# Optimization experiments

Measured on AMD Instinct MI355X. Metric: run time of the kernel, lower is better.

## Reference

```python
import jax, jax.numpy as jnp
import numpy as np

B, N, C, H = 8, 1024, 1024, 16
D = C // H
SCALE = D ** -0.5


def setup_inputs() -> dict:
    key = jax.random.key(0)
    ks = jax.random.split(key, 5)
    s = 0.02  # keep pre-softmax logits in a sane range
    return {
        "x": jax.random.normal(ks[0], (B, N, C), dtype=jnp.float32),
        "Wq": jax.random.normal(ks[1], (C, C), dtype=jnp.float32) * s,
        "bq": jax.random.normal(ks[2], (C,), dtype=jnp.float32) * s,
        "Wkv": jax.random.normal(ks[3], (C, 2 * C), dtype=jnp.float32) * s,
        "bkv": jax.random.normal(ks[4], (2 * C,), dtype=jnp.float32) * s,
    }


def reference(x, Wq, bq, Wkv, bkv):
    b, n, c = x.shape
    h, d = H, c // H
    q = (x @ Wq + bq).reshape(b, n, h, d)                 # [b,n,h,d]
    kv = x @ Wkv + bkv                                     # [b,n,2c]
    k, v = jnp.split(kv, 2, axis=-1)                       # each [b,n,c]
    k = k.reshape(b, n, h, d)
    v = v.reshape(b, n, h, d)
    att = jnp.einsum("bnhd,bmhd->bnmh", q, k) * SCALE      # [b,n,m,h]
    att = jax.nn.softmax(att, axis=2)                      # softmax over keys (m)
    out = jnp.einsum("bnmh,bmhd->bnhd", att, v).reshape(b, n, c)
    return out
```

## Files before the change

### kernel.cpp

```cpp
#include <hip/hip_runtime.h>
#include <stdint.h>

using u16 = unsigned short;
using u32 = unsigned int;
using bf16x8 = __attribute__((ext_vector_type(8))) __bf16;
using f32x4  = __attribute__((ext_vector_type(4))) float;

#define NB 8
#define NN 1024
#define NC 1024
#define NH 16
#define ND 64
#define QSCALE 0.18033688011112042f

__device__ __forceinline__ u16 f2bf(float f) {
  u32 u = __float_as_uint(f);
  return (u16)((u + 0x7fffu + ((u >> 16) & 1u)) >> 16);
}
__device__ __forceinline__ u16 bfc(float f) {
  __bf16 b = (__bf16)f;
  return __builtin_bit_cast(u16, b);
}
__device__ __forceinline__ u32 pack2(u16 a, u16 b) { return (u32)a | ((u32)b << 16); }

__device__ __forceinline__ void gload16(const void* g, void* l) {
  __builtin_amdgcn_global_load_lds((__attribute__((address_space(1))) const u32*)g,
                                   (__attribute__((address_space(3))) u32*)l, 16, 0, 0);
}

__global__ void k_prep(const float* __restrict__ x, const float* __restrict__ Wq,
                       const float* __restrict__ bq, const float* __restrict__ Wkv,
                       const float* __restrict__ bkv,
                       u16* __restrict__ xb, u16* __restrict__ Wt, float* __restrict__ bias) {
  __shared__ u16 tile[64][72];
  int bid = blockIdx.x;
  int t = threadIdx.x;
  if (bid < 8192) {
    int i = bid * 256 + t;
    float4 v = ((const float4*)x)[i];
    ((uint2*)xb)[i] = make_uint2(pack2(f2bf(v.x), f2bf(v.y)), pack2(f2bf(v.z), f2bf(v.w)));
    return;
  }
  if (bid < 8960) {
    int pb = bid - 8192;
    int k0 = (pb & 15) << 6;
    int c0 = (pb >> 4) << 6;
    bool isQ = (c0 < 1024);
    const float* src = isQ ? Wq : Wkv;
    int ldw  = isQ ? 1024 : 2048;
    int csrc = isQ ? c0 : (c0 - 1024);
    float sc = isQ ? QSCALE : 1.0f;

    int r  = t >> 2;
    int cq = (t & 3) << 4;
    const float* p = src + (size_t)(k0 + r) * ldw + csrc + cq;
#pragma unroll
    for (int j = 0; j < 16; j += 4) {
      float4 v = *(const float4*)(p + j);
      tile[r][cq + j + 0] = f2bf(v.x * sc);
      tile[r][cq + j + 1] = f2bf(v.y * sc);
      tile[r][cq + j + 2] = f2bf(v.z * sc);
      tile[r][cq + j + 3] = f2bf(v.w * sc);
    }
    __syncthreads();
    int co = t >> 2;
    int kq = (t & 3) << 4;
    u16 v0[16];
#pragma unroll
    for (int j = 0; j < 16; ++j) v0[j] = tile[kq + j][co];
    uint4 o0, o1;
    o0.x = pack2(v0[0], v0[1]);  o0.y = pack2(v0[2], v0[3]);
    o0.z = pack2(v0[4], v0[5]);  o0.w = pack2(v0[6], v0[7]);
    o1.x = pack2(v0[8], v0[9]);  o1.y = pack2(v0[10], v0[11]);
    o1.z = pack2(v0[12], v0[13]); o1.w = pack2(v0[14], v0[15]);
    u16* dst = Wt + (size_t)(c0 + co) * 1024 + k0 + kq;
    *(uint4*)dst = o0;
    *(uint4*)(dst + 8) = o1;
    return;
  }
  {
    int i = (bid - 8960) * 256 + t;
    if (i < 1024) bias[i] = bq[i] * QSCALE;
    else if (i < 3072) bias[i] = bkv[i - 1024];
  }
}

__launch_bounds__(512, 4)
__global__ void k_gemm(const u16* __restrict__ A, const u16* __restrict__ Bw,
                       const float* __restrict__ bias,
                       u16* __restrict__ qws, u16* __restrict__ kws, u16* __restrict__ vtw) {
  __shared__ __align__(16) u16 Ab[2][4096];
  __shared__ __align__(16) u16 Bb[2][8192];
  int flat = blockIdx.x;
  int swz = (flat & 7) * 96 + (flat >> 3);
  int m0 = (swz & 63) * 128;
  int n0 = (swz >> 6) * 256;
  int tid = threadIdx.x;
  int w = tid >> 6, lane = tid & 63;
  int lo = lane & 15, hi = lane >> 4;
  int wm = w >> 2, wn = w & 3;

  f32x4 acc[4][4] = {};

  int srow = tid >> 2;
  int schunk = (tid & 3) ^ ((tid >> 3) & 3);
  const u16* Ag  = A  + (size_t)(m0 + srow) * 1024 + schunk * 8;
  const u16* Bg0 = Bw + (size_t)(n0 + srow) * 1024 + schunk * 8;
  const u16* Bg1 = Bw + (size_t)(n0 + 128 + srow) * 1024 + schunk * 8;

  int ck = ((hi ^ ((lo >> 1) & 3)) << 3);

#define STAGE(BUF, KO)                                  \
  gload16(Ag  + (KO), &Ab[BUF][tid * 8]);               \
  gload16(Bg0 + (KO), &Bb[BUF][tid * 8]);               \
  gload16(Bg1 + (KO), &Bb[BUF][4096 + tid * 8]);

  STAGE(0, 0);
  __syncthreads();

  for (int t = 0; t < 32; ++t) {
    int cb = t & 1;
    if (t < 31) { STAGE(cb ^ 1, (t + 1) * 32); }
    bf16x8 af[4], bfr[4];
#pragma unroll
    for (int mi = 0; mi < 4; ++mi)
      af[mi] = *(const bf16x8*)&Ab[cb][(wm * 64 + mi * 16 + lo) * 32 + ck];
#pragma unroll
    for (int ni = 0; ni < 4; ++ni)
      bfr[ni] = *(const bf16x8*)&Bb[cb][(wn * 64 + ni * 16 + lo) * 32 + ck];
#pragma unroll
    for (int mi = 0; mi < 4; ++mi)
#pragma unroll
      for (int ni = 0; ni < 4; ++ni)
        acc[mi][ni] = __builtin_amdgcn_mfma_f32_16x16x32_bf16(af[mi], bfr[ni], acc[mi][ni], 0, 0, 0);
    __syncthreads();
  }
#undef STAGE

#pragma unroll
  for (int ni = 0; ni < 4; ++ni) {
    int c = n0 + wn * 64 + ni * 16 + lo;
    float bvl = bias[c];
    if (c < 2048) {
#pragma unroll
      for (int mi = 0; mi < 4; ++mi) {
#pragma unroll
        for (int r = 0; r < 4; ++r) {
          int m = m0 + wm * 64 + mi * 16 + hi * 4 + r;
          int b = m >> 10, tok = m & 1023;
          u16 o = f2bf(acc[mi][ni][r] + bvl);
          if (c < 1024) {
            int h = c >> 6, d = c & 63;
            qws[((size_t)(b * 16 + h) * 1024 + tok) * 64 + d] = o;
          } else {
            int c2 = c - 1024; int h = c2 >> 6, d = c2 & 63;
            kws[((size_t)(b * 16 + h) * 1024 + tok) * 64 + d] = o;
          }
        }
      }
    } else {
      int c2 = c - 2048; int h = c2 >> 6, d = c2 & 63;
#pragma unroll
      for (int mi = 0; mi < 4; ++mi) {
        int m = m0 + wm * 64 + mi * 16 + hi * 4;
        int b = m >> 10, tok = m & 1023;
        ushort4 pk;
        pk.x = bfc(acc[mi][ni][0] + bvl);
        pk.y = bfc(acc[mi][ni][1] + bvl);
        pk.z = bfc(acc[mi][ni][2] + bvl);
        pk.w = bfc(acc[mi][ni][3] + bvl);
        *(ushort4*)&vtw[((size_t)(b * 16 + h) * 64 + d) * 1024 + tok] = pk;
      }
    }
  }
}

__launch_bounds__(512)
__global__ void k_attn(const u16* __restrict__ q, const u16* __restrict__ k,
                       const u16* __restrict__ vt, float* __restrict__ out) {
  __shared__ __align__(16) u16 Ks[2][4096];
  __shared__ __align__(16) u16 Vs[2][4096];
  __shared__ __align__(16) u16 P[8][16][72];
  int bh = blockIdx.x;
  int q0 = blockIdx.y * 128;
  int tid = threadIdx.x;
  int w = tid >> 6, lane = tid & 63;
  int lo = lane & 15, hi = lane >> 4;
  int b = bh >> 4, h = bh & 15;

  const u16* kbase = k  + (size_t)bh * 65536;
  const u16* vbase = vt + (size_t)bh * 65536;

  int srow = w * 8 + (lane >> 3);
  int cg   = (lane & 7) ^ ((lane >> 3) & 7);
  const u16* gK = kbase + (size_t)srow * 64   + cg * 8;
  const u16* gV = vbase + (size_t)srow * 1024 + cg * 8;
  u16* lK0 = &Ks[0][w * 512];
  u16* lK1 = &Ks[1][w * 512];
  u16* lV0 = &Vs[0][w * 512];
  u16* lV1 = &Vs[1][w * 512];

  const u16* qp = q + ((size_t)bh * 1024 + q0 + w * 16 + lo) * 64 + hi * 8;
  bf16x8 qf0 = *(const bf16x8*)(qp);
  bf16x8 qf1 = *(const bf16x8*)(qp + 32);

  f32x4 acc_o[4] = {};
  float m_s = -1e30f;
  float l_s = 0.f;

  int sw = lo & 7;

  gload16(gK, lK0);
  gload16(gV, lV0);
  __syncthreads();

  for (int t = 0; t < 16; ++t) {
    int cur = t & 1;
    if (t < 15) {
      gload16(gK + (t + 1) * 4096, cur ? lK0 : lK1);
      gload16(gV + (t + 1) * 64,   cur ? lV0 : lV1);
    }
    f32x4 s[4] = {};
    const u16* kb = Ks[cur];
#pragma unroll
    for (int ni = 0; ni < 4; ++ni) {
      const u16* kp = kb + (ni * 16 + lo) * 64;
      bf16x8 kf0 = *(const bf16x8*)(kp + ((hi ^ sw) * 8));
      bf16x8 kf1 = *(const bf16x8*)(kp + (((4 + hi) ^ sw) * 8));
      s[ni] = __builtin_amdgcn_mfma_f32_16x16x32_bf16(kf0, qf0, s[ni], 0, 0, 0);
      s[ni] = __builtin_amdgcn_mfma_f32_16x16x32_bf16(kf1, qf1, s[ni], 0, 0, 0);
    }
    float pm;
    {
      float a0 = fmaxf(fmaxf(s[0][0], s[0][1]), fmaxf(s[0][2], s[0][3]));
      float a1 = fmaxf(fmaxf(s[1][0], s[1][1]), fmaxf(s[1][2], s[1][3]));
      float a2 = fmaxf(fmaxf(s[2][0], s[2][1]), fmaxf(s[2][2], s[2][3]));
      float a3 = fmaxf(fmaxf(s[3][0], s[3][1]), fmaxf(s[3][2], s[3][3]));
      pm = fmaxf(fmaxf(a0, a1), fmaxf(a2, a3));
      pm = fmaxf(pm, __shfl_xor(pm, 16));
      pm = fmaxf(pm, __shfl_xor(pm, 32));
    }
    if (!__all(pm <= m_s + 8.0f)) {
      float mn = fmaxf(m_s, pm);
      float corr = __builtin_amdgcn_exp2f(m_s - mn);
      m_s = mn;
      l_s *= corr;
      float cr[4];
#pragma unroll
      for (int r = 0; r < 4; ++r) cr[r] = __shfl(corr, hi * 4 + r);
#pragma unroll
      for (int ci = 0; ci < 4; ++ci)
#pragma unroll
        for (int r = 0; r < 4; ++r) acc_o[ci][r] *= cr[r];
    }
    float rs = 0.f;
#pragma unroll
    for (int ni = 0; ni < 4; ++ni) {
      float p0 = __builtin_amdgcn_exp2f(s[ni][0] - m_s);
      float p1 = __builtin_amdgcn_exp2f(s[ni][1] - m_s);
      float p2 = __builtin_amdgcn_exp2f(s[ni][2] - m_s);
      float p3 = __builtin_amdgcn_exp2f(s[ni][3] - m_s);
      rs += (p0 + p1) + (p2 + p3);
      ushort4 pk;
      pk.x = bfc(p0); pk.y = bfc(p1); pk.z = bfc(p2); pk.w = bfc(p3);
      *(ushort4*)&P[w][lo][ni * 16 + hi * 4] = pk;
    }
    rs += __shfl_xor(rs, 16);
    rs += __shfl_xor(rs, 32);
    l_s += rs;
    bf16x8 pf0 = *(const bf16x8*)(&P[w][lo][hi * 8]);
    bf16x8 pf1 = *(const bf16x8*)(&P[w][lo][32 + hi * 8]);
    const u16* vb = Vs[cur];
#pragma unroll
    for (int ci = 0; ci < 4; ++ci) {
      const u16* vp = vb + (ci * 16 + lo) * 64;
      bf16x8 vf0 = *(const bf16x8*)(vp + ((hi ^ sw) * 8));
      bf16x8 vf1 = *(const bf16x8*)(vp + (((4 + hi) ^ sw) * 8));
      acc_o[ci] = __builtin_amdgcn_mfma_f32_16x16x32_bf16(pf0, vf0, acc_o[ci], 0, 0, 0);
      acc_o[ci] = __builtin_amdgcn_mfma_f32_16x16x32_bf16(pf1, vf1, acc_o[ci], 0, 0, 0);
    }
    __syncthreads();
  }
  float inv = 1.0f / l_s;
  float ivr[4];
#pragma unroll
  for (int r = 0; r < 4; ++r) ivr[r] = __shfl(inv, hi * 4 + r);
#pragma unroll
  for (int r = 0; r < 4; ++r) {
    int n = q0 + w * 16 + hi * 4 + r;
    float* dst = out + ((size_t)(b * 1024 + n)) * 1024 + h * 64;
#pragma unroll
    for (int ci = 0; ci < 4; ++ci) dst[ci * 16 + lo] = acc_o[ci][r] * ivr[r];
  }
}

extern "C" void kernel_launch(void* const* d_in, const int* in_sizes, int n_in,
                              void* d_out, int out_size, void* d_ws, size_t ws_size,
                              hipStream_t stream) {
  const float* x   = (const float*)d_in[0];
  const float* Wq  = (const float*)d_in[1];
  const float* bq  = (const float*)d_in[2];
  const float* Wkv = (const float*)d_in[3];
  const float* bkv = (const float*)d_in[4];
  float* out = (float*)d_out;

  char* ws = (char*)d_ws;
  u16*   xb   = (u16*)(ws);
  u16*   Wt   = (u16*)(ws + 16777216);
  float* bias = (float*)(ws + 23068672);
  u16*   qws  = (u16*)(ws + 23080960);
  u16*   kws  = (u16*)(ws + 39858176);
  u16*   vtw  = (u16*)(ws + 73412608);

  k_prep<<<8972, 256, 0, stream>>>(x, Wq, bq, Wkv, bkv, xb, Wt, bias);
  k_gemm<<<768, 512, 0, stream>>>(xb, Wt, bias, qws, kws, vtw);
  {
    dim3 g(128, 8);
    k_attn<<<g, 512, 0, stream>>>(qws, kws, vtw, out);
  }
}
```

Measured before the change: 139.4 us.

## Triple-buffer projection GEMM with split-phase loads, barriers and MFMA priority

Replaces the double-buffered K-loop of the QKV projection GEMM with a three-stage LDS ring. Each K-tile is split into two MFMA halves, with the A and B global loads for a later tile issued between them. Explicit vmcnt waits, s_barrier plus sched_barrier, and s_setprio around MFMA bursts aim to overlap global-to-LDS traffic with matrix math and let waves interleave better. The cost is 50% more LDS per block, which may reduce resident blocks per CU, plus more barriers per tile.

```diff
diff --git a/kernel.cpp b/kernel.cpp
--- a/kernel.cpp
+++ b/kernel.cpp
@@ -89,8 +89,8 @@
 __global__ void k_gemm(const u16* __restrict__ A, const u16* __restrict__ Bw,
                        const float* __restrict__ bias,
                        u16* __restrict__ qws, u16* __restrict__ kws, u16* __restrict__ vtw) {
-  __shared__ __align__(16) u16 Ab[2][4096];
-  __shared__ __align__(16) u16 Bb[2][8192];
+  __shared__ __align__(16) u16 RA[3][4096];
+  __shared__ __align__(16) u16 RB[3][8192];
   int flat = blockIdx.x;
   int swz = (flat & 7) * 96 + (flat >> 3);
   int m0 = (swz & 63) * 128;
@@ -110,32 +110,68 @@
 
   int ck = ((hi ^ ((lo >> 1) & 3)) << 3);
 
-#define STAGE(BUF, KO)                                  \
-  gload16(Ag  + (KO), &Ab[BUF][tid * 8]);               \
-  gload16(Bg0 + (KO), &Bb[BUF][tid * 8]);               \
-  gload16(Bg1 + (KO), &Bb[BUF][4096 + tid * 8]);
-
-  STAGE(0, 0);
-  __syncthreads();
-
-  for (int t = 0; t < 32; ++t) {
-    int cb = t & 1;
-    if (t < 31) { STAGE(cb ^ 1, (t + 1) * 32); }
-    bf16x8 af[4], bfr[4];
-#pragma unroll
-    for (int mi = 0; mi < 4; ++mi)
-      af[mi] = *(const bf16x8*)&Ab[cb][(wm * 64 + mi * 16 + lo) * 32 + ck];
-#pragma unroll
-    for (int ni = 0; ni < 4; ++ni)
-      bfr[ni] = *(const bf16x8*)&Bb[cb][(wn * 64 + ni * 16 + lo) * 32 + ck];
-#pragma unroll
-    for (int mi = 0; mi < 4; ++mi)
-#pragma unroll
-      for (int ni = 0; ni < 4; ++ni)
-        acc[mi][ni] = __builtin_amdgcn_mfma_f32_16x16x32_bf16(af[mi], bfr[ni], acc[mi][ni], 0, 0, 0);
-    __syncthreads();
-  }
-#undef STAGE
+#define MFMA_(a, b, c) __builtin_amdgcn_mfma_f32_16x16x32_bf16(a, b, c, 0, 0, 0)
+#define SBAR() __builtin_amdgcn_s_barrier(); __builtin_amdgcn_sched_barrier(0)
+
+#define TILE(S, SN, DOST, KT, VM0)                                            \
+  {                                                                           \
+    bf16x8 af[4], bfr[4];                                                     \
+    if (DOST) gload16(Ag + (size_t)(KT) * 32, &RA[SN][tid * 8]);              \
+    _Pragma("unroll")                                                         \
+    for (int mi = 0; mi < 4; ++mi)                                            \
+      af[mi] = *(const bf16x8*)&RA[S][(wm * 64 + mi * 16 + lo) * 32 + ck];    \
+    _Pragma("unroll")                                                         \
+    for (int ni = 0; ni < 2; ++ni)                                            \
+      bfr[ni] = *(const bf16x8*)&RB[S][(wn * 64 + ni * 16 + lo) * 32 + ck];   \
+    SBAR();                                                                   \
+    __builtin_amdgcn_s_setprio(1);                                            \
+    _Pragma("unroll")                                                         \
+    for (int mi = 0; mi < 4; ++mi)                                            \
+      _Pragma("unroll")                                                       \
+      for (int ni = 0; ni < 2; ++ni)                                          \
+        acc[mi][ni] = MFMA_(af[mi], bfr[ni], acc[mi][ni]);                    \
+    __builtin_amdgcn_s_setprio(0);                                            \
+    SBAR();                                                                   \
+    if (DOST) {                                                               \
+      gload16(Bg0 + (size_t)(KT) * 32, &RB[SN][tid * 8]);                     \
+      gload16(Bg1 + (size_t)(KT) * 32, &RB[SN][4096 + tid * 8]);              \
+    }                                                                         \
+    _Pragma("unroll")                                                         \
+    for (int ni = 2; ni < 4; ++ni)                                            \
+      bfr[ni] = *(const bf16x8*)&RB[S][(wn * 64 + ni * 16 + lo) * 32 + ck];   \
+    if (VM0) { asm volatile("s_waitcnt vmcnt(0)" ::: "memory"); }             \
+    else     { asm volatile("s_waitcnt vmcnt(3)" ::: "memory"); }             \
+    SBAR();                                                                   \
+    __builtin_amdgcn_s_setprio(1);                                            \
+    _Pragma("unroll")                                                         \
+    for (int mi = 0; mi < 4; ++mi)                                            \
+      _Pragma("unroll")                                                       \
+      for (int ni = 2; ni < 4; ++ni)                                          \
+        acc[mi][ni] = MFMA_(af[mi], bfr[ni], acc[mi][ni]);                    \
+    __builtin_amdgcn_s_setprio(0);                                            \
+    SBAR();                                                                   \
+  }
+
+  gload16(Ag,       &RA[0][tid * 8]);
+  gload16(Bg0,      &RB[0][tid * 8]);
+  gload16(Bg1,      &RB[0][4096 + tid * 8]);
+  gload16(Ag + 32,  &RA[1][tid * 8]);
+  gload16(Bg0 + 32, &RB[1][tid * 8]);
+  gload16(Bg1 + 32, &RB[1][4096 + tid * 8]);
+  asm volatile("s_waitcnt vmcnt(3)" ::: "memory");
+  SBAR();
+
+#pragma unroll 1
+  for (int u = 0; u < 30; u += 3) {
+    TILE(0, 2, true, u + 2, false);
+    TILE(1, 0, true, u + 3, false);
+    TILE(2, 1, true, u + 4, false);
+  }
+  TILE(0, 2, false, 0, true);
+  TILE(1, 0, false, 0, false);
+#undef TILE
+#undef SBAR
+#undef MFMA_
 
 #pragma unroll
   for (int ni = 0; ni < 4; ++ni) {
```

Result: no change. 139.1 us (-0.2%).

## Enlarge QKV GEMM tile to 256x256 with K=64 staging and interleaved MFMA schedule

Applied to the files above, without the earlier changes.

The projection GEMM moves from 128x256 tiles with K=32 steps to 256x256 tiles with K=64 steps, halving the grid to 384 blocks and doubling each wave's accumulator footprint. Global-to-LDS loads for the next tiles are interleaved between four MFMA quadrants, with explicit barriers, lgkm/vmcnt waits and s_setprio to overlap memory with compute. The aim is more reuse per loaded byte and fewer loop iterations and barriers. The cost is heavier register and LDS pressure (occupancy hint drops to 2) and only 384 blocks to spread across the CUs.

```diff
diff --git a/kernel.cpp b/kernel.cpp
--- a/kernel.cpp
+++ b/kernel.cpp
@@ -85,57 +85,136 @@
   }
 }
 
-__launch_bounds__(512, 4)
+__launch_bounds__(512, 2)
 __global__ void k_gemm(const u16* __restrict__ A, const u16* __restrict__ Bw,
                        const float* __restrict__ bias,
                        u16* __restrict__ qws, u16* __restrict__ kws, u16* __restrict__ vtw) {
-  __shared__ __align__(16) u16 Ab[2][4096];
-  __shared__ __align__(16) u16 Bb[2][8192];
+  __shared__ __align__(16) u16 LA[2][16384];
+  __shared__ __align__(16) u16 LB[2][16384];
   int flat = blockIdx.x;
-  int swz = (flat & 7) * 96 + (flat >> 3);
-  int m0 = (swz & 63) * 128;
-  int n0 = (swz >> 6) * 256;
+  int swz = (flat & 7) * 48 + (flat >> 3);
+  int m0 = (swz & 31) * 256;
+  int n0 = (swz >> 5) * 256;
   int tid = threadIdx.x;
   int w = tid >> 6, lane = tid & 63;
   int lo = lane & 15, hi = lane >> 4;
   int wm = w >> 2, wn = w & 3;
 
-  f32x4 acc[4][4] = {};
-
-  int srow = tid >> 2;
-  int schunk = (tid & 3) ^ ((tid >> 3) & 3);
-  const u16* Ag  = A  + (size_t)(m0 + srow) * 1024 + schunk * 8;
-  const u16* Bg0 = Bw + (size_t)(n0 + srow) * 1024 + schunk * 8;
-  const u16* Bg1 = Bw + (size_t)(n0 + 128 + srow) * 1024 + schunk * 8;
-
-  int ck = ((hi ^ ((lo >> 1) & 3)) << 3);
-
-#define STAGE(BUF, KO)                                  \
-  gload16(Ag  + (KO), &Ab[BUF][tid * 8]);               \
-  gload16(Bg0 + (KO), &Bb[BUF][tid * 8]);               \
-  gload16(Bg1 + (KO), &Bb[BUF][4096 + tid * 8]);
-
-  STAGE(0, 0);
-  __syncthreads();
-
-  for (int t = 0; t < 32; ++t) {
-    int cb = t & 1;
-    if (t < 31) { STAGE(cb ^ 1, (t + 1) * 32); }
-    bf16x8 af[4], bfr[4];
-#pragma unroll
-    for (int mi = 0; mi < 4; ++mi)
-      af[mi] = *(const bf16x8*)&Ab[cb][(wm * 64 + mi * 16 + lo) * 32 + ck];
-#pragma unroll
-    for (int ni = 0; ni < 4; ++ni)
-      bfr[ni] = *(const bf16x8*)&Bb[cb][(wn * 64 + ni * 16 + lo) * 32 + ck];
-#pragma unroll
-    for (int mi = 0; mi < 4; ++mi)
-#pragma unroll
-      for (int ni = 0; ni < 4; ++ni)
-        acc[mi][ni] = __builtin_amdgcn_mfma_f32_16x16x32_bf16(af[mi], bfr[ni], acc[mi][ni], 0, 0, 0);
-    __syncthreads();
-  }
-#undef STAGE
+  f32x4 acc[8][4] = {};
+
+  int cs = ((tid & 7) ^ ((tid >> 3) & 7)) * 8;
+  const u16* Ag = A  + (size_t)(m0 + (tid >> 3)) * 1024 + cs;
+  const u16* Bg = Bw + (size_t)(n0 + (tid >> 3)) * 1024 + cs;
+
+  int ck0 = ((hi ^ (lo & 7)) << 3);
+  int ck1 = (((4 + hi) ^ (lo & 7)) << 3);
+  const u16* laR = &LA[0][wm * 8192 + lo * 64];
+  const u16* lbR = &LB[0][(wn >> 1) * 8192 + ((wn & 1) * 64 + lo) * 64];
+
+#define MFMA_(a, b, c) __builtin_amdgcn_mfma_f32_16x16x32_bf16(a, b, c, 0, 0, 0)
+#define SBAR() __builtin_amdgcn_sched_barrier(0); __builtin_amdgcn_s_barrier(); __builtin_amdgcn_sched_barrier(0)
+#define LGKM0() asm volatile("s_waitcnt lgkmcnt(0)" ::: "memory"); __builtin_amdgcn_sched_barrier(0)
+
+#define ST_A(BUF, MH, KT)                                                                   \
+  gload16(Ag + (size_t)((MH) * 128) * 1024 + (KT) * 64,      &LA[BUF][(MH) * 8192 + tid * 8]); \
+  gload16(Ag + (size_t)((MH) * 128 + 64) * 1024 + (KT) * 64, &LA[BUF][(MH) * 8192 + 4096 + tid * 8]);
+#define ST_B(BUF, NH, KT)                                                                   \
+  gload16(Bg + (size_t)((NH) * 128) * 1024 + (KT) * 64,      &LB[BUF][(NH) * 8192 + tid * 8]); \
+  gload16(Bg + (size_t)((NH) * 128 + 64) * 1024 + (KT) * 64, &LB[BUF][(NH) * 8192 + 4096 + tid * 8]);
+
+  ST_A(0, 0, 0); ST_A(0, 1, 0); ST_B(0, 0, 0); ST_B(0, 1, 0);
+  ST_A(1, 0, 1); ST_A(1, 1, 1); ST_B(1, 0, 1);
+  asm volatile("s_waitcnt vmcnt(6)" ::: "memory");
+  __builtin_amdgcn_s_barrier();
+
+#pragma unroll 1
+  for (int t = 0; t < 16; ++t) {
+    int b = t & 1;
+    const u16* la = laR + b * 16384;
+    const u16* lb = lbR + b * 16384;
+    bf16x8 af[4][2], bf0[2][2], bf1[2][2];
+
+#pragma unroll
+    for (int mi = 0; mi < 4; ++mi) {
+      af[mi][0] = *(const bf16x8*)(la + mi * 1024 + ck0);
+      af[mi][1] = *(const bf16x8*)(la + mi * 1024 + ck1);
+    }
+#pragma unroll
+    for (int ni = 0; ni < 2; ++ni) {
+      bf0[ni][0] = *(const bf16x8*)(lb + ni * 1024 + ck0);
+      bf0[ni][1] = *(const bf16x8*)(lb + ni * 1024 + ck1);
+    }
+    if (t < 15) { ST_B(b ^ 1, 1, t + 1); }
+    SBAR();
+    LGKM0();
+    __builtin_amdgcn_s_setprio(1);
+#pragma unroll
+    for (int ks = 0; ks < 2; ++ks)
+#pragma unroll
+      for (int mi = 0; mi < 4; ++mi)
+#pragma unroll
+        for (int ni = 0; ni < 2; ++ni)
+          acc[mi][ni] = MFMA_(af[mi][ks], bf0[ni][ks], acc[mi][ni]);
+    __builtin_amdgcn_s_setprio(0);
+    SBAR();
+
+#pragma unroll
+    for (int ni = 0; ni < 2; ++ni) {
+      bf1[ni][0] = *(const bf16x8*)(lb + (2 + ni) * 1024 + ck0);
+      bf1[ni][1] = *(const bf16x8*)(lb + (2 + ni) * 1024 + ck1);
+    }
+    SBAR();
+    LGKM0();
+    __builtin_amdgcn_s_setprio(1);
+#pragma unroll
+    for (int ks = 0; ks < 2; ++ks)
+#pragma unroll
+      for (int mi = 0; mi < 4; ++mi)
+#pragma unroll
+        for (int ni = 0; ni < 2; ++ni)
+          acc[mi][2 + ni] = MFMA_(af[mi][ks], bf1[ni][ks], acc[mi][2 + ni]);
+    __builtin_amdgcn_s_setprio(0);
+    SBAR();
+
+#pragma unroll
+    for (int mi = 0; mi < 4; ++mi) {
+      af[mi][0] = *(const bf16x8*)(la + (4 + mi) * 1024 + ck0);
+      af[mi][1] = *(const bf16x8*)(la + (4 + mi) * 1024 + ck1);
+    }
+    if (t < 14) { ST_B(b, 0, t + 2); }
+    SBAR();
+    LGKM0();
+    __builtin_amdgcn_s_setprio(1);
+#pragma unroll
+    for (int ks = 0; ks < 2; ++ks)
+#pragma unroll
+      for (int mi = 0; mi < 4; ++mi)
+#pragma unroll
+        for (int ni = 0; ni < 2; ++ni)
+          acc[4 + mi][ni] = MFMA_(af[mi][ks], bf0[ni][ks], acc[4 + mi][ni]);
+    __builtin_amdgcn_s_setprio(0);
+    SBAR();
+
+    if (t < 14) { ST_A(b, 0, t + 2); ST_A(b, 1, t + 2); }
+    SBAR();
+    __builtin_amdgcn_s_setprio(1);
+#pragma unroll
+    for (int ks = 0; ks < 2; ++ks)
+#pragma unroll
+      for (int mi = 0; mi < 4; ++mi)
+#pragma unroll
+        for (int ni = 0; ni < 2; ++ni)
+          acc[4 + mi][2 + ni] = MFMA_(af[mi][ks], bf1[ni][ks], acc[4 + mi][2 + ni]);
+    __builtin_amdgcn_s_setprio(0);
+    if (t < 14)       { asm volatile("s_waitcnt vmcnt(6)" ::: "memory"); }
+    else if (t == 14) { asm volatile("s_waitcnt vmcnt(0)" ::: "memory"); }
+    SBAR();
+  }
+#undef ST_A
+#undef ST_B
+#undef SBAR
+#undef LGKM0
+#undef MFMA_
 
 #pragma unroll
   for (int ni = 0; ni < 4; ++ni) {
@@ -143,10 +222,10 @@
     float bvl = bias[c];
     if (c < 2048) {
 #pragma unroll
-      for (int mi = 0; mi < 4; ++mi) {
+      for (int mi = 0; mi < 8; ++mi) {
 #pragma unroll
         for (int r = 0; r < 4; ++r) {
-          int m = m0 + wm * 64 + mi * 16 + hi * 4 + r;
+          int m = m0 + wm * 128 + mi * 16 + hi * 4 + r;
           int b = m >> 10, tok = m & 1023;
           u16 o = f2bf(acc[mi][ni][r] + bvl);
           if (c < 1024) {
@@ -161,8 +240,8 @@
     } else {
       int c2 = c - 2048; int h = c2 >> 6, d = c2 & 63;
 #pragma unroll
-      for (int mi = 0; mi < 4; ++mi) {
-        int m = m0 + wm * 64 + mi * 16 + hi * 4;
+      for (int mi = 0; mi < 8; ++mi) {
+        int m = m0 + wm * 128 + mi * 16 + hi * 4;
         int b = m >> 10, tok = m & 1023;
         ushort4 pk;
         pk.x = bfc(acc[mi][ni][0] + bvl);
@@ -313,7 +392,7 @@
   u16*   vtw  = (u16*)(ws + 73412608);
 
   k_prep<<<8972, 256, 0, stream>>>(x, Wq, bq, Wkv, bkv, xb, Wt, bias);
-  k_gemm<<<768, 512, 0, stream>>>(xb, Wt, bias, qws, kws, vtw);
+  k_gemm<<<384, 512, 0, stream>>>(xb, Wt, bias, qws, kws, vtw);
   {
     dim3 g(128, 8);
     k_attn<<<g, 512, 0, stream>>>(qws, kws, vtw, out);
```

Result: slower. 146.7 us (+5.2%).
